# Performance work log

Measured on AMD Instinct MI355X. Metric: run time of the kernel, lower is better.

Reference implementation:

```python
import jax, jax.numpy as jnp
import numpy as np

N_NODES = 100000
BN_EPS = 1e-5


def gcn_conv(x, W, b, row, col, n_nodes):
    """GCNConv: D^{-1/2}(A+I)D^{-1/2} X W + b, edges row->col."""
    h = x @ W  # [N, out]
    # degree with self-loops, counted on destination side (symmetric for undirected)
    deg = jax.ops.segment_sum(jnp.ones(row.shape[0], dtype=x.dtype), col,
                              num_segments=n_nodes) + 1.0
    dis = jax.lax.rsqrt(deg)  # deg^{-1/2}
    coef = dis[row] * dis[col]  # [E]
    msg = h[row] * coef[:, None]  # gather + scale, [E, out]
    agg = jax.ops.segment_sum(msg, col, num_segments=n_nodes)
    # self-loop contribution: norm = dis[i]*dis[i]
    out = agg + h * (dis * dis)[:, None] + b
    return out


def batchnorm_train(x, gamma, beta):
    mean = jnp.mean(x, axis=0)
    var = jnp.mean(jnp.square(x - mean), axis=0)  # biased, training mode
    return (x - mean) * jax.lax.rsqrt(var + BN_EPS) * gamma + beta


def setup_inputs() -> dict:
    key = jax.random.key(0)
    ks = jax.random.split(key, 8)
    latent_dim, hidden_dim, input_dim = 64, 128, 128
    n_edges = 1600000
    x = jax.random.normal(ks[0], (N_NODES, latent_dim), dtype=jnp.float32)
    edge_index = jax.random.randint(ks[1], (2, n_edges), 0, N_NODES, dtype=jnp.int64)
    s1 = 1.0 / np.sqrt(latent_dim)
    s2 = 1.0 / np.sqrt(hidden_dim)
    W1 = jax.random.uniform(ks[2], (latent_dim, hidden_dim), jnp.float32, -s1, s1)
    b1 = jax.random.uniform(ks[3], (hidden_dim,), jnp.float32, -s1, s1)
    gamma = jnp.ones((hidden_dim,), jnp.float32)
    beta = jnp.zeros((hidden_dim,), jnp.float32)
    W2 = jax.random.uniform(ks[4], (hidden_dim, input_dim), jnp.float32, -s2, s2)
    b2 = jax.random.uniform(ks[5], (input_dim,), jnp.float32, -s2, s2)
    return {"quantized_f_embedding": x, "edge_index": edge_index,
            "W1": W1, "b1": b1, "gamma": gamma, "beta": beta,
            "W2": W2, "b2": b2}


def reference(quantized_f_embedding, edge_index, W1, b1, gamma, beta, W2, b2):
    row, col = edge_index[0], edge_index[1]
    h = gcn_conv(quantized_f_embedding, W1, b1, row, col, N_NODES)
    h = batchnorm_train(h, gamma, beta)
    out = gcn_conv(h, W2, b2, row, col, N_NODES)
    return out
```

## Files before the change

kernel.cpp:

```cpp
#include <hip/hip_runtime.h>

#define NN 100000
#define BN_EPS 1e-5f
#define NB 391
#define CAP 5120
#define TILE 4096

#define NREP 16
#define CVT_BLKS 6250
#define AGG_BLKS 6250
#define ZERO_BLKS 48
#define PACK1_BLKS 32

typedef __attribute__((ext_vector_type(4))) _Float16 half4;
typedef __attribute__((ext_vector_type(8))) _Float16 half8;
typedef __attribute__((ext_vector_type(4))) float f32x4;


__global__ __launch_bounds__(256) void k_prep0(int* __restrict__ bcur,
                                               float* __restrict__ stats,
                                               const float* __restrict__ W1,
                                               _Float16* __restrict__ wp1) {
    const int b = blockIdx.x;
    const int t = threadIdx.x;
    if (b < ZERO_BLKS) {
        int i = b * 256 + t;
        if (i < 8192) bcur[i] = 0;
        else stats[i - 8192] = 0.f;
    } else {
        int i = (b - ZERO_BLKS) * 256 + t;
        int j = i & 7, l = (i >> 3) & 63, nt = (i >> 9) & 7, kt = i >> 12;
        int k = kt * 32 + ((l >> 4) << 3) + j;
        int n = nt * 16 + (l & 15);
        wp1[i] = (_Float16)W1[k * 128 + n];
    }
}


__global__ __launch_bounds__(256) void k_binc(const int* __restrict__ row,
                                              const int* __restrict__ col,
                                              int* __restrict__ bcur,
                                              int* __restrict__ ebuf,
                                              int E, int binBlks,
                                              const float* __restrict__ x,
                                              _Float16* __restrict__ xh) {
    __shared__ int hist[512];
    __shared__ int excl[512];
    __shared__ int cur[512];
    __shared__ int gbase[512];
    __shared__ int sc[256];
    __shared__ int staged[TILE];
    __shared__ unsigned short bkt[TILE];
    const int t = threadIdx.x;

    if (blockIdx.x >= binBlks) {
        int i = (blockIdx.x - binBlks) * 256 + t;
        float4 v = reinterpret_cast<const float4*>(x)[i];
        half4 o;
        o.x = (_Float16)v.x; o.y = (_Float16)v.y;
        o.z = (_Float16)v.z; o.w = (_Float16)v.w;
        reinterpret_cast<half4*>(xh)[i] = o;
        return;
    }

    const int base = blockIdx.x * TILE;
    const int nE = min(TILE, E - base);

    hist[t] = 0; hist[t + 256] = 0;
    cur[t] = 0;  cur[t + 256] = 0;
    __syncthreads();

    int er[16], ec[16];
    #pragma unroll
    for (int k = 0; k < 16; ++k) {
        int idx = base + k * 256 + t;
        if (idx < E) {
            er[k] = row[idx];
            ec[k] = col[idx];
            atomicAdd(&hist[ec[k] >> 8], 1);
        } else {
            ec[k] = -1;
        }
    }
    __syncthreads();

    int p = hist[2 * t] + hist[2 * t + 1];
    sc[t] = p;
    __syncthreads();
    for (int off = 1; off < 256; off <<= 1) {
        int add = (t >= off) ? sc[t - off] : 0;
        __syncthreads();
        sc[t] += add;
        __syncthreads();
    }
    int P = sc[t];
    excl[2 * t]     = P - p;
    excl[2 * t + 1] = P - p + hist[2 * t];
    __syncthreads();

    for (int b = t; b < NB; b += 256) {
        int h = hist[b];
        gbase[b] = h ? atomicAdd(&bcur[b * 16], h) : 0;
    }

    #pragma unroll
    for (int k = 0; k < 16; ++k) {
        int c = ec[k];
        if (c < 0) continue;
        int b = c >> 8;
        int slot = excl[b] + atomicAdd(&cur[b], 1);
        staged[slot] = (er[k] << 8) | (c & 255);
        bkt[slot] = (unsigned short)b;
    }
    __syncthreads();

    for (int i = t; i < nE; i += 256) {
        int b = bkt[i];
        int off = gbase[b] + (i - excl[b]);
        if (off < CAP) ebuf[b * CAP + off] = staged[i];
    }
}


__global__ __launch_bounds__(256) void k_csr(const int* __restrict__ bcur,
                                             const int* __restrict__ ebuf,
                                             int* __restrict__ rows,
                                             int* __restrict__ start,
                                             int* __restrict__ cnt,
                                             float* __restrict__ dis) {
    __shared__ int hist[256];
    __shared__ int lstart[256];
    __shared__ int cur[256];
    __shared__ int sc[256];
    const int b = blockIdx.x;
    const int t = threadIdx.x;
    const int fill = min(bcur[b * 16], CAP);

    hist[t] = 0; cur[t] = 0;
    __syncthreads();

    int er[CAP / 256];
    #pragma unroll
    for (int k = 0; k < CAP / 256; ++k) {
        int i = k * 256 + t;
        if (i < fill) {
            er[k] = ebuf[b * CAP + i];
            atomicAdd(&hist[er[k] & 255], 1);
        }
    }
    __syncthreads();

    int v = hist[t];
    sc[t] = v;
    __syncthreads();
    for (int off = 1; off < 256; off <<= 1) {
        int add = (t >= off) ? sc[t - off] : 0;
        __syncthreads();
        sc[t] += add;
        __syncthreads();
    }
    lstart[t] = sc[t] - v;

    const int node = b * 256 + t;
    if (node < NN) {
        start[node] = b * CAP + lstart[t];
        cnt[node] = v;
        dis[node] = rsqrtf((float)(v + 1));
    }
    __syncthreads();

    #pragma unroll
    for (int k = 0; k < CAP / 256; ++k) {
        int i = k * 256 + t;
        if (i < fill) {
            int lc = er[k] & 255;
            int lpos = atomicAdd(&cur[lc], 1);
            rows[b * CAP + lstart[lc] + lpos] = er[k] >> 8;
        }
    }
}


__device__ __forceinline__ void fma_h4(float4& a, half4 v, float c) {
    a.x = fmaf((float)v.x, c, a.x);
    a.y = fmaf((float)v.y, c, a.y);
    a.z = fmaf((float)v.z, c, a.z);
    a.w = fmaf((float)v.w, c, a.w);
}

template<bool SUMC>
__device__ __forceinline__ void agg_body(int blk,
                                         const _Float16* __restrict__ xh,
                                         const int* __restrict__ rows,
                                         const int* __restrict__ start,
                                         const int* __restrict__ cnt,
                                         const float* __restrict__ dis,
                                         _Float16* __restrict__ agg,
                                         float* __restrict__ sumcoef) {
    constexpr int L = 16;
    const int t = threadIdx.x;
    const int g = t / L;
    const int fid = t % L;
    const int n = blk * 16 + g;
    if (n >= NN) return;
    const int s = start[n];
    const int c = cnt[n];
    const float dn = dis[n];
    const half4* X4 = reinterpret_cast<const half4*>(xh);
    half4 hv = X4[n * L + fid];
    const float dn2 = dn * dn;
    float4 acc = make_float4(dn2 * (float)hv.x, dn2 * (float)hv.y,
                             dn2 * (float)hv.z, dn2 * (float)hv.w);
    float sd = 0.f;
    const int* rp = rows + s;
    int k = 0;
    for (; k + 4 <= c; k += 4) {
        int r0 = rp[k], r1 = rp[k + 1], r2 = rp[k + 2], r3 = rp[k + 3];
        float d0 = dis[r0], d1 = dis[r1], d2 = dis[r2], d3 = dis[r3];
        half4 v0 = X4[r0 * L + fid];
        half4 v1 = X4[r1 * L + fid];
        half4 v2 = X4[r2 * L + fid];
        half4 v3 = X4[r3 * L + fid];
        fma_h4(acc, v0, d0 * dn);
        fma_h4(acc, v1, d1 * dn);
        fma_h4(acc, v2, d2 * dn);
        fma_h4(acc, v3, d3 * dn);
        sd += (d0 + d1) + (d2 + d3);
    }
    for (; k < c; ++k) {
        int r = rp[k];
        float dr = dis[r];
        half4 v = X4[r * L + fid];
        fma_h4(acc, v, dr * dn);
        sd += dr;
    }
    half4 o;
    o.x = (_Float16)acc.x; o.y = (_Float16)acc.y;
    o.z = (_Float16)acc.z; o.w = (_Float16)acc.w;
    reinterpret_cast<half4*>(agg)[n * L + fid] = o;
    if (SUMC && fid == 0) sumcoef[n] = dn * sd + dn2;
}


__device__ __forceinline__ void l2prep_body(int bb,
                                            const float* __restrict__ stats,
                                            const float* __restrict__ gamma,
                                            const float* __restrict__ beta,
                                            const float* __restrict__ b1,
                                            const float* __restrict__ W1,
                                            const float* __restrict__ W2,
                                            _Float16* __restrict__ wp12,
                                            float* __restrict__ sv) {
    __shared__ float s_[128];
    __shared__ float f2_[128];
    const int t = threadIdx.x;
    if (t < 128) {
        float sum = 0.f, sum2 = 0.f;
        #pragma unroll
        for (int r = 0; r < NREP; ++r) {
            sum  += stats[r * 256 + t];
            sum2 += stats[r * 256 + 128 + t];
        }
        const float n = (float)NN;
        float mean = sum / n;
        float var = sum2 / n - mean * mean;
        float sc = gamma[t] * rsqrtf(var + BN_EPS);
        s_[t] = sc;
        f2_[t] = b1[t] * sc + (beta[t] - mean * sc);
    }
    __syncthreads();
    if (bb < 32) {
        int i = bb * 256 + t;
        int j = i & 7, l = (i >> 3) & 63, nt = (i >> 9) & 7, kt = i >> 12;
        int kk = kt * 32 + ((l >> 4) << 3) + j;
        int nn = nt * 16 + (l & 15);
        float acc = 0.f;
        #pragma unroll 8
        for (int m = 0; m < 128; ++m)
            acc = fmaf(W1[kk * 128 + m] * s_[m], W2[m * 128 + nn], acc);
        wp12[i] = (_Float16)acc;
    } else if (t < 128) {
        float acc = 0.f;
        for (int k = 0; k < 128; ++k) acc = fmaf(f2_[k], W2[k * 128 + t], acc);
        sv[t] = acc;
    }
}


__global__ __launch_bounds__(256) void k_aggy(const _Float16* __restrict__ xh,
                                              const int* __restrict__ rows,
                                              const int* __restrict__ start,
                                              const int* __restrict__ cnt,
                                              const float* __restrict__ dis,
                                              _Float16* __restrict__ agg,
                                              float* __restrict__ sumcoef) {
    agg_body<true>(blockIdx.x, xh, rows, start, cnt, dis, agg, sumcoef);
}


__global__ __launch_bounds__(256) void k_aggz(const _Float16* __restrict__ y,
                                              const int* __restrict__ rows,
                                              const int* __restrict__ start,
                                              const int* __restrict__ cnt,
                                              const float* __restrict__ dis,
                                              _Float16* __restrict__ z,
                                              const float* __restrict__ stats,
                                              const float* __restrict__ gamma,
                                              const float* __restrict__ beta,
                                              const float* __restrict__ b1,
                                              const float* __restrict__ W1,
                                              const float* __restrict__ W2,
                                              _Float16* __restrict__ wp12,
                                              float* __restrict__ sv) {
    if (blockIdx.x < AGG_BLKS) {
        agg_body<false>(blockIdx.x, y, rows, start, cnt, dis, z, nullptr);
    } else {
        l2prep_body(blockIdx.x - AGG_BLKS, stats, gamma, beta, b1, W1, W2,
                    wp12, sv);
    }
}


template<bool FINAL>
__global__ __launch_bounds__(256) void k_mgemm(const _Float16* __restrict__ A,
                                               const _Float16* __restrict__ Wp,
                                               const float* __restrict__ bias,
                                               const float* __restrict__ sv,
                                               const float* __restrict__ sumcoef,
                                               float* __restrict__ out32,
                                               float* __restrict__ stats) {
    const int t = threadIdx.x;
    const int wv = t >> 6;
    const int ln = t & 63;
    const int cgrp = ln >> 4;
    const int ncol = ln & 15;
    const int r0 = blockIdx.x * 64 + wv * 16;
    const int arow = min(r0 + ncol, NN - 1);

    f32x4 acc[8];
    #pragma unroll
    for (int nt = 0; nt < 8; ++nt) acc[nt] = {0.f, 0.f, 0.f, 0.f};

    const half8* Ap = reinterpret_cast<const half8*>(A + arow * 64 + cgrp * 8);
    const half8* Bp = reinterpret_cast<const half8*>(Wp);

    #pragma unroll
    for (int kt = 0; kt < 2; ++kt) {
        half8 a = Ap[kt * 4];
        #pragma unroll
        for (int nt = 0; nt < 8; ++nt) {
            half8 b = Bp[(kt * 8 + nt) * 64 + ln];
            acc[nt] = __builtin_amdgcn_mfma_f32_16x16x32_f16(a, b, acc[nt], 0, 0, 0);
        }
    }

    if constexpr (!FINAL) {
        __shared__ float ls[4][128];
        __shared__ float ls2[4][128];
        #pragma unroll
        for (int nt = 0; nt < 8; ++nt) {
            const int n = nt * 16 + ncol;
            const float bn = bias[n];
            float s = 0.f, s2 = 0.f;
            #pragma unroll
            for (int j = 0; j < 4; ++j) {
                int gr = r0 + cgrp * 4 + j;
                float v = acc[nt][j] + bn;
                if (gr < NN) {
                    s += v;
                    s2 += v * v;
                }
            }
            s  += __shfl_xor(s, 16);  s  += __shfl_xor(s, 32);
            s2 += __shfl_xor(s2, 16); s2 += __shfl_xor(s2, 32);
            if (ln < 16) { ls[wv][n] = s; ls2[wv][n] = s2; }
        }
        __syncthreads();
        float* rep = stats + (blockIdx.x & (NREP - 1)) * 256;
        if (t < 128) {
            atomicAdd(&rep[t], ls[0][t] + ls[1][t] + ls[2][t] + ls[3][t]);
        } else {
            int u = t - 128;
            atomicAdd(&rep[128 + u], ls2[0][u] + ls2[1][u] + ls2[2][u] + ls2[3][u]);
        }
    } else {
        float scj[4];
        #pragma unroll
        for (int j = 0; j < 4; ++j) scj[j] = sumcoef[min(r0 + cgrp * 4 + j, NN - 1)];
        #pragma unroll
        for (int nt = 0; nt < 8; ++nt) {
            const int n = nt * 16 + ncol;
            const float svn = sv[n];
            const float bn = bias[n];
            #pragma unroll
            for (int j = 0; j < 4; ++j) {
                int gr = r0 + cgrp * 4 + j;
                if (gr < NN) out32[gr * 128 + n] = acc[nt][j] + scj[j] * svn + bn;
            }
        }
    }
}


extern "C" void kernel_launch(void* const* d_in, const int* in_sizes, int n_in,
                              void* d_out, int out_size, void* d_ws, size_t ws_size,
                              hipStream_t stream) {
    const float* x     = (const float*)d_in[0];
    const int*   ei    = (const int*)d_in[1];
    const float* W1    = (const float*)d_in[2];
    const float* b1    = (const float*)d_in[3];
    const float* gamma = (const float*)d_in[4];
    const float* beta  = (const float*)d_in[5];
    const float* W2    = (const float*)d_in[6];
    const float* b2    = (const float*)d_in[7];
    float* out = (float*)d_out;

    const int E = in_sizes[1] / 2;
    const int* row = ei;
    const int* col = ei + E;
    const int binBlks = (E + TILE - 1) / TILE;

    int*   bcur    = (int*)d_ws;
    int*   cnt     = bcur + 8192;
    int*   start   = cnt + 102400;
    float* dis     = (float*)(start + 102400);
    float* stats   = dis + 102400;
    float* sv      = stats + 4096;
    float* sumcoef = stats + 5120;
    _Float16* wp1  = (_Float16*)(sumcoef + 102400);
    _Float16* wp12 = wp1 + 8192;
    int*   rows    = (int*)(wp12 + 8192);
    int*   Rbase   = rows + NB * CAP;
    _Float16* xh   = (_Float16*)Rbase;
    int*   ebuf    = Rbase + 3276800;
    _Float16* y    = (_Float16*)(ebuf + NB * CAP);
    _Float16* z    = xh;

    k_prep0<<<ZERO_BLKS + PACK1_BLKS, 256, 0, stream>>>(bcur, stats, W1, wp1);
    k_binc<<<binBlks + CVT_BLKS, 256, 0, stream>>>(row, col, bcur, ebuf, E,
                                                   binBlks, x, xh);
    k_csr<<<NB, 256, 0, stream>>>(bcur, ebuf, rows, start, cnt, dis);

    k_aggy<<<AGG_BLKS, 256, 0, stream>>>(xh, rows, start, cnt, dis, y, sumcoef);
    k_mgemm<false><<<(NN + 63) / 64, 256, 0, stream>>>(y, wp1, b1, nullptr,
                                                       nullptr, nullptr, stats);

    k_aggz<<<AGG_BLKS + 33, 256, 0, stream>>>(y, rows, start, cnt, dis, z,
                                              stats, gamma, beta, b1, W1, W2,
                                              wp12, sv);

    k_mgemm<true><<<(NN + 63) / 64, 256, 0, stream>>>(z, wp12, b2, sv,
                                                      sumcoef, out, nullptr);
}
```

Baseline: 148.4 us.

## Halve CSR bucket width to 128 nodes and stage final GEMM stores via LDS

Edge binning now uses 782 buckets of 128 destination nodes, each capped at 2560 edges, in place of 391 buckets of 256. The aim is more CSR-build blocks and fewer edges per block, so that kernel gets more parallelism and less per-block LDS atomic work. The final GEMM epilogue now stages results in shared memory and writes coalesced float4 rows instead of scattered scalar stores. The trade-offs are a larger shared histogram in the binning kernel, tighter per-bucket capacity that could drop edges on skewed degree distributions, and extra shared memory plus a barrier in the GEMM.

```diff
diff --git a/kernel.cpp b/kernel.cpp
--- a/kernel.cpp
+++ b/kernel.cpp
@@ -2,14 +2,14 @@
 
 #define NN 100000
 #define BN_EPS 1e-5f
-#define NB 391
-#define CAP 5120
+#define NBK 782
+#define CAP 2560
 #define TILE 4096
 
 #define NREP 16
 #define CVT_BLKS 6250
 #define AGG_BLKS 6250
-#define ZERO_BLKS 48
+#define ZERO_BLKS 80
 #define PACK1_BLKS 32
 
 typedef __attribute__((ext_vector_type(4))) _Float16 half4;
@@ -25,8 +25,8 @@
     const int t = threadIdx.x;
     if (b < ZERO_BLKS) {
         int i = b * 256 + t;
-        if (i < 8192) bcur[i] = 0;
-        else stats[i - 8192] = 0.f;
+        if (i < 16384) bcur[i] = 0;
+        else stats[i - 16384] = 0.f;
     } else {
         int i = (b - ZERO_BLKS) * 256 + t;
         int j = i & 7, l = (i >> 3) & 63, nt = (i >> 9) & 7, kt = i >> 12;
@@ -44,10 +44,10 @@
                                               int E, int binBlks,
                                               const float* __restrict__ x,
                                               _Float16* __restrict__ xh) {
-    __shared__ int hist[512];
-    __shared__ int excl[512];
-    __shared__ int cur[512];
-    __shared__ int gbase[512];
+    __shared__ int hist[1024];
+    __shared__ int excl[1024];
+    __shared__ int cur[1024];
+    __shared__ int gbase[1024];
     __shared__ int sc[256];
     __shared__ int staged[TILE];
     __shared__ unsigned short bkt[TILE];
@@ -66,8 +66,8 @@
     const int base = blockIdx.x * TILE;
     const int nE = min(TILE, E - base);
 
-    hist[t] = 0; hist[t + 256] = 0;
-    cur[t] = 0;  cur[t + 256] = 0;
+    #pragma unroll
+    for (int q = 0; q < 4; ++q) { hist[q * 256 + t] = 0; cur[q * 256 + t] = 0; }
     __syncthreads();
 
     int er[16], ec[16];
@@ -77,14 +77,15 @@
         if (idx < E) {
             er[k] = row[idx];
             ec[k] = col[idx];
-            atomicAdd(&hist[ec[k] >> 8], 1);
+            atomicAdd(&hist[ec[k] >> 7], 1);
         } else {
             ec[k] = -1;
         }
     }
     __syncthreads();
 
-    int p = hist[2 * t] + hist[2 * t + 1];
+    int h0 = hist[4 * t], h1 = hist[4 * t + 1], h2 = hist[4 * t + 2], h3 = hist[4 * t + 3];
+    int p = h0 + h1 + h2 + h3;
     sc[t] = p;
     __syncthreads();
     for (int off = 1; off < 256; off <<= 1) {
@@ -93,12 +94,14 @@
         sc[t] += add;
         __syncthreads();
     }
-    int P = sc[t];
-    excl[2 * t]     = P - p;
-    excl[2 * t + 1] = P - p + hist[2 * t];
-    __syncthreads();
-
-    for (int b = t; b < NB; b += 256) {
+    int e0 = sc[t] - p;
+    excl[4 * t]     = e0;
+    excl[4 * t + 1] = e0 + h0;
+    excl[4 * t + 2] = e0 + h0 + h1;
+    excl[4 * t + 3] = e0 + h0 + h1 + h2;
+    __syncthreads();
+
+    for (int b = t; b < NBK; b += 256) {
         int h = hist[b];
         gbase[b] = h ? atomicAdd(&bcur[b * 16], h) : 0;
     }
@@ -107,9 +110,9 @@
     for (int k = 0; k < 16; ++k) {
         int c = ec[k];
         if (c < 0) continue;
-        int b = c >> 8;
+        int b = c >> 7;
         int slot = excl[b] + atomicAdd(&cur[b], 1);
-        staged[slot] = (er[k] << 8) | (c & 255);
+        staged[slot] = (er[k] << 7) | (c & 127);
         bkt[slot] = (unsigned short)b;
     }
     __syncthreads();
@@ -128,15 +131,15 @@
                                              int* __restrict__ start,
                                              int* __restrict__ cnt,
                                              float* __restrict__ dis) {
-    __shared__ int hist[256];
-    __shared__ int lstart[256];
-    __shared__ int cur[256];
+    __shared__ int hist[128];
+    __shared__ int lstart[128];
+    __shared__ int cur[128];
     __shared__ int sc[256];
     const int b = blockIdx.x;
     const int t = threadIdx.x;
     const int fill = min(bcur[b * 16], CAP);
 
-    hist[t] = 0; cur[t] = 0;
+    if (t < 128) { hist[t] = 0; cur[t] = 0; }
     __syncthreads();
 
     int er[CAP / 256];
@@ -145,12 +148,12 @@
         int i = k * 256 + t;
         if (i < fill) {
             er[k] = ebuf[b * CAP + i];
-            atomicAdd(&hist[er[k] & 255], 1);
-        }
-    }
-    __syncthreads();
-
-    int v = hist[t];
+            atomicAdd(&hist[er[k] & 127], 1);
+        }
+    }
+    __syncthreads();
+
+    int v = (t < 128) ? hist[t] : 0;
     sc[t] = v;
     __syncthreads();
     for (int off = 1; off < 256; off <<= 1) {
@@ -159,13 +162,14 @@
         sc[t] += add;
         __syncthreads();
     }
-    lstart[t] = sc[t] - v;
-
-    const int node = b * 256 + t;
-    if (node < NN) {
-        start[node] = b * CAP + lstart[t];
-        cnt[node] = v;
-        dis[node] = rsqrtf((float)(v + 1));
+    if (t < 128) {
+        lstart[t] = sc[t] - v;
+        const int node = b * 128 + t;
+        if (node < NN) {
+            start[node] = b * CAP + (sc[t] - v);
+            cnt[node] = v;
+            dis[node] = rsqrtf((float)(v + 1));
+        }
     }
     __syncthreads();
 
@@ -173,9 +177,9 @@
     for (int k = 0; k < CAP / 256; ++k) {
         int i = k * 256 + t;
         if (i < fill) {
-            int lc = er[k] & 255;
+            int lc = er[k] & 127;
             int lpos = atomicAdd(&cur[lc], 1);
-            rows[b * CAP + lstart[lc] + lpos] = er[k] >> 8;
+            rows[b * CAP + lstart[lc] + lpos] = er[k] >> 7;
         }
     }
 }
@@ -384,6 +388,7 @@
             atomicAdd(&rep[128 + u], ls2[0][u] + ls2[1][u] + ls2[2][u] + ls2[3][u]);
         }
     } else {
+        __shared__ float st[4][16][132];
         float scj[4];
         #pragma unroll
         for (int j = 0; j < 4; ++j) scj[j] = sumcoef[min(r0 + cgrp * 4 + j, NN - 1)];
@@ -393,9 +398,19 @@
             const float svn = sv[n];
             const float bn = bias[n];
             #pragma unroll
-            for (int j = 0; j < 4; ++j) {
-                int gr = r0 + cgrp * 4 + j;
-                if (gr < NN) out32[gr * 128 + n] = acc[nt][j] + scj[j] * svn + bn;
+            for (int j = 0; j < 4; ++j)
+                st[wv][cgrp * 4 + j][n] = acc[nt][j] + scj[j] * svn + bn;
+        }
+        __syncthreads();
+        #pragma unroll
+        for (int i = 0; i < 8; ++i) {
+            int idx = i * 64 + ln;
+            int rr = idx >> 5;
+            int c4 = idx & 31;
+            int gr = r0 + rr;
+            if (gr < NN) {
+                float4 v = *reinterpret_cast<float4*>(&st[wv][rr][c4 * 4]);
+                *reinterpret_cast<float4*>(&out32[gr * 128 + c4 * 4]) = v;
             }
         }
     }
@@ -421,7 +436,7 @@
     const int binBlks = (E + TILE - 1) / TILE;
 
     int*   bcur    = (int*)d_ws;
-    int*   cnt     = bcur + 8192;
+    int*   cnt     = bcur + 16384;
     int*   start   = cnt + 102400;
     float* dis     = (float*)(start + 102400);
     float* stats   = dis + 102400;
@@ -430,16 +445,16 @@
     _Float16* wp1  = (_Float16*)(sumcoef + 102400);
     _Float16* wp12 = wp1 + 8192;
     int*   rows    = (int*)(wp12 + 8192);
-    int*   Rbase   = rows + NB * CAP;
+    int*   Rbase   = rows + NBK * CAP;
     _Float16* xh   = (_Float16*)Rbase;
     int*   ebuf    = Rbase + 3276800;
-    _Float16* y    = (_Float16*)(ebuf + NB * CAP);
+    _Float16* y    = (_Float16*)(ebuf + NBK * CAP);
     _Float16* z    = xh;
 
     k_prep0<<<ZERO_BLKS + PACK1_BLKS, 256, 0, stream>>>(bcur, stats, W1, wp1);
     k_binc<<<binBlks + CVT_BLKS, 256, 0, stream>>>(row, col, bcur, ebuf, E,
                                                    binBlks, x, xh);
-    k_csr<<<NB, 256, 0, stream>>>(bcur, ebuf, rows, start, cnt, dis);
+    k_csr<<<NBK, 256, 0, stream>>>(bcur, ebuf, rows, start, cnt, dis);
 
     k_aggy<<<AGG_BLKS, 256, 0, stream>>>(xh, rows, start, cnt, dis, y, sumcoef);
     k_mgemm<false><<<(NN + 63) / 64, 256, 0, stream>>>(y, wp1, b1, nullptr,
```

New measurement: 147.6 us (median of 3 runs). About the same (-0.5%).
